# Performance work log

Measured on AMD Instinct MI355X. Metric: run time of the kernel, lower is better.

The kernel has to match this reference:

```python
import jax, jax.numpy as jnp
import numpy as np

N, C, H, W = 64, 512, 32, 32
HID, NCLS = 240, 10


def setup_inputs() -> dict:
    key = jax.random.key(0)
    ks = jax.random.split(key, 6)
    d = {
        "x": jax.random.normal(ks[0], (N, C, H, W), jnp.float32),
        "bn1_g": jnp.ones((C,), jnp.float32),
        "bn1_b": jnp.zeros((C,), jnp.float32),
        "bn1_m": jnp.zeros((C,), jnp.float32),
        "bn1_v": jnp.ones((C,), jnp.float32),
        "conv1_w": jax.random.normal(ks[1], (C, C, 3, 3), jnp.float32) * 0.02,
        "bn2_g": jnp.ones((C,), jnp.float32),
        "bn2_b": jnp.zeros((C,), jnp.float32),
        "bn2_m": jnp.zeros((C,), jnp.float32),
        "bn2_v": jnp.ones((C,), jnp.float32),
        "conv2_w": jax.random.normal(ks[2], (C, C, 3, 3), jnp.float32) * 0.02,
        "fc1_w": jax.random.normal(ks[3], (HID, C), jnp.float32) * 0.05,
        "fc1_b": jnp.zeros((HID,), jnp.float32),
        "fc2_w": jax.random.normal(ks[4], (NCLS, HID), jnp.float32) * 0.05,
        "fc2_b": jnp.zeros((NCLS,), jnp.float32),
    }
    return d


def _bn(x, g, b, m, v, eps=1e-5):
    # eval-mode BatchNorm2d, NCHW
    inv = g / jnp.sqrt(v + eps)
    return x * inv[None, :, None, None] + (b - m * inv)[None, :, None, None]


def _conv3(x, w):
    return jax.lax.conv_general_dilated(
        x, w, window_strides=(1, 1), padding="SAME",
        dimension_numbers=("NCHW", "OIHW", "NCHW"))


def _probe(feat, fc1_w, fc1_b, fc2_w, fc2_b):
    # Global_Avg_Flatten -> Linear -> Softplus(beta=5) -> Linear
    g = feat.mean(axis=(2, 3))                       # (N, C)
    h = jax.nn.softplus(5.0 * (g @ fc1_w.T + fc1_b)) / 5.0  # (N, HID)
    return h @ fc2_w.T + fc2_b                       # (N, NCLS)


def _get_mask(feat, fc1_w, fc1_b, fc2_w, fc2_b):
    # eval branch: sum of top-1 + top-2 logits, grad wrt (detached) feat
    feat_sg = jax.lax.stop_gradient(feat)

    def logit_sum(f_):
        logits = _probe(f_, fc1_w, fc1_b, fc2_w, fc2_b)
        idx = jax.lax.top_k(logits, 2)[1]            # (N, 2) int indices
        return jnp.take_along_axis(logits, idx, axis=1).sum()

    g = jax.grad(logit_sum)(feat_sg)                 # (N, C, H, W)
    # adaptive_avg_pool2d(.,1)*H*W == spatial sum
    s = g.sum(axis=(2, 3))                           # (N, C)
    m = jax.nn.softmax(s, axis=1) * 2.0
    return m[:, :, None, None]


def reference(x, bn1_g, bn1_b, bn1_m, bn1_v, conv1_w,
              bn2_g, bn2_b, bn2_m, bn2_v, conv2_w,
              fc1_w, fc1_b, fc2_w, fc2_b):
    out1 = jax.nn.relu(_bn(x, bn1_g, bn1_b, bn1_m, bn1_v))  # equalInOut path
    mask = _get_mask(out1, fc1_w, fc1_b, fc2_w, fc2_b)
    pred_probe = _probe(out1, fc1_w, fc1_b, fc2_w, fc2_b)
    masked = out1 * mask
    h = jax.nn.relu(_bn(_conv3(masked, conv1_w), bn2_g, bn2_b, bn2_m, bn2_v))
    h = _conv3(h, conv2_w)
    out = x + h
    return (out, pred_probe)
```

## Files before the change

### kernel.cpp

```cpp
#include <hip/hip_runtime.h>
#include <stdint.h>

typedef __bf16 bf16x8 __attribute__((ext_vector_type(8)));
typedef float f32x4v __attribute__((ext_vector_type(4)));

typedef __attribute__((address_space(1))) const void gconst_t;
typedef __attribute__((address_space(3))) void lds_t;

#define GLL16(gp, sp) __builtin_amdgcn_global_load_lds((gconst_t*)(uintptr_t)(gp), (lds_t*)(uintptr_t)(sp), 16, 0, 0)

__device__ __forceinline__ unsigned short f2bf(float f) {
  unsigned int u = __float_as_uint(f);
  u = (u + 0x7FFFu + ((u >> 16) & 1u)) >> 16;
  return (unsigned short)u;
}
__device__ __forceinline__ float bf2f(unsigned int b) {
  return __uint_as_float(b << 16);
}

#define SPP 1156

__global__ __launch_bounds__(512) void bnprep(
    const float* __restrict__ g1, const float* __restrict__ b1,
    const float* __restrict__ m1, const float* __restrict__ v1,
    const float* __restrict__ g2, const float* __restrict__ b2,
    const float* __restrict__ m2, const float* __restrict__ v2,
    float* __restrict__ bnp) {
  int t = threadIdx.x;
  float i1 = g1[t] * rsqrtf(v1[t] + 1e-5f);
  bnp[t] = i1;
  bnp[512 + t] = b1[t] - m1[t] * i1;
  float i2 = g2[t] * rsqrtf(v2[t] + 1e-5f);
  bnp[1024 + t] = i2;
  bnp[1536 + t] = b2[t] - m2[t] * i2;
}

__global__ __launch_bounds__(256) void ring_zero(unsigned short* __restrict__ Ap,
                                                 unsigned short* __restrict__ Hp) {
  const int n = blockIdx.y;
  const int p = blockIdx.x * 4 + (threadIdx.x >> 6);
  const int lane = threadIdx.x & 63;
  int y, x;
  if (p < 34) { y = 0; x = p; }
  else if (p < 68) { y = 33; x = p - 34; }
  else if (p < 100) { y = p - 67; x = 0; }
  else { y = p - 99; x = 33; }
  const uint4 z = {0u, 0u, 0u, 0u};
  const size_t off = ((size_t)((n * 34 + y) * 34 + x)) * 512 + lane * 8;
  *(uint4*)(Ap + off) = z;
  *(uint4*)(Hp + off) = z;
}

__global__ __launch_bounds__(256) void wtrans(const float* __restrict__ w1, const float* __restrict__ w2,
                                              unsigned short* __restrict__ w1t, unsigned short* __restrict__ w2t) {
  unsigned e = blockIdx.x * 256u + threadIdx.x;
  if (e >= 4718592u) return;
  const float* w = (e < 2359296u) ? w1 : w2;
  unsigned short* o = (e < 2359296u) ? w1t : w2t;
  unsigned r = (e < 2359296u) ? e : (e - 2359296u);
  unsigned ci = r & 511u, co = (r >> 9) & 511u, tt = r >> 18;
  o[r] = f2bf(w[(co * 512u + ci) * 9u + tt]);
}

__global__ __launch_bounds__(256) void bn1_relu_stage(const float* __restrict__ x, const float* __restrict__ bnp,
                                                      unsigned short* __restrict__ Ap, float* __restrict__ partial) {
  int bid = blockIdx.x;
  int n = bid >> 6, ciblk = (bid >> 3) & 7, yblk = bid & 7;
  int ci0 = ciblk * 64, y0 = yblk * 4;
  int t = threadIdx.x;
  __shared__ __align__(16) float vals[64 * 128];
  __shared__ float ivs[64], bbs[64];
  if (t < 64) { ivs[t] = bnp[ci0 + t]; bbs[t] = bnp[512 + ci0 + t]; }
  __syncthreads();
#pragma unroll
  for (int i = 0; i < 8; ++i) {
    int f4 = i * 256 + t;
    int cil = f4 >> 5, xq = f4 & 31;
    const float* src = x + ((size_t)(n * 512 + ci0 + cil)) * 1024 + y0 * 32 + xq * 4;
    f32x4v v = *(const f32x4v*)src;
    float iv = ivs[cil], bb = bbs[cil];
    f32x4v r;
    r[0] = fmaxf(fmaf(v[0], iv, bb), 0.f);
    r[1] = fmaxf(fmaf(v[1], iv, bb), 0.f);
    r[2] = fmaxf(fmaf(v[2], iv, bb), 0.f);
    r[3] = fmaxf(fmaf(v[3], iv, bb), 0.f);
    *(f32x4v*)&vals[cil * 128 + xq * 4] = r;
  }
  __syncthreads();
  {
    int cil = t >> 2, q = t & 3;
    float s = 0.f;
#pragma unroll
    for (int j = 0; j < 32; ++j) s += vals[cil * 128 + q * 32 + j];
    s += __shfl_xor(s, 1);
    s += __shfl_xor(s, 2);
    if (q == 0) partial[((size_t)n * 512 + ci0 + cil) * 8 + yblk] = s;
  }
  {
    int yx = t >> 1, half = t & 1;
    int y = y0 + (yx >> 5), xx = yx & 31;
    unsigned short* dp = Ap + ((size_t)((n * 34 + y + 1) * 34 + (xx + 1))) * 512 + ci0 + half * 32;
    unsigned wrd[16];
#pragma unroll
    for (int j = 0; j < 16; ++j) {
      unsigned lo = f2bf(vals[(half * 32 + 2 * j) * 128 + yx]);
      unsigned hi = f2bf(vals[(half * 32 + 2 * j + 1) * 128 + yx]);
      wrd[j] = lo | (hi << 16);
    }
#pragma unroll
    for (int k = 0; k < 4; ++k) {
      uint4 u;
      u.x = wrd[k * 4]; u.y = wrd[k * 4 + 1]; u.z = wrd[k * 4 + 2]; u.w = wrd[k * 4 + 3];
      *(uint4*)(dp + k * 8) = u;
    }
  }
}

__global__ __launch_bounds__(256) void probe_mask(const float* __restrict__ partial,
                                                  const float* __restrict__ fc1w, const float* __restrict__ fc1b,
                                                  const float* __restrict__ fc2w, const float* __restrict__ fc2b,
                                                  float* __restrict__ maskp, float* __restrict__ probeout) {
  int n = blockIdx.x, t = threadIdx.x;
  int lane = t & 63, wv = t >> 6;
  __shared__ float gl[512], sl[512], zl[240], hl[240], dzl[240], logl[10], red[4];
  __shared__ int idx2[2];
  for (int c = t; c < 512; c += 256) {
    const float* pp = partial + ((size_t)n * 512 + c) * 8;
    float s = 0.f;
#pragma unroll
    for (int j = 0; j < 8; ++j) s += pp[j];
    gl[c] = s * (1.f / 1024.f);
  }
  __syncthreads();
  if (t < 240) {
    float z = fc1b[t];
    const float* wr = fc1w + t * 512;
    for (int c = 0; c < 512; ++c) z = fmaf(gl[c], wr[c], z);
    zl[t] = z;
    float u = 5.f * z;
    float sp = (u > 20.f) ? u : log1pf(expf(u));
    hl[t] = sp * 0.2f;
  }
  __syncthreads();
  if (t < 10) {
    float L = fc2b[t];
    const float* wr = fc2w + t * 240;
    for (int h = 0; h < 240; ++h) L = fmaf(hl[h], wr[h], L);
    logl[t] = L;
    probeout[n * 10 + t] = L;
  }
  __syncthreads();
  if (t == 0) {
    float b1v = -1e30f, b2v = -1e30f; int i1 = 0, i2 = 0;
    for (int j = 0; j < 10; ++j) {
      float v = logl[j];
      if (v > b1v) { b2v = b1v; i2 = i1; b1v = v; i1 = j; }
      else if (v > b2v) { b2v = v; i2 = j; }
    }
    idx2[0] = i1; idx2[1] = i2;
  }
  __syncthreads();
  if (t < 240) {
    float dh = fc2w[idx2[0] * 240 + t] + fc2w[idx2[1] * 240 + t];
    float u = 5.f * zl[t];
    float sg = 1.f / (1.f + expf(-u));
    dzl[t] = dh * sg;
  }
  __syncthreads();
  for (int c = t; c < 512; c += 256) {
    float s = 0.f;
    for (int h = 0; h < 240; ++h) s = fmaf(dzl[h], fc1w[h * 512 + c], s);
    sl[c] = s;
  }
  __syncthreads();
  float m = fmaxf(sl[t], sl[t + 256]);
#pragma unroll
  for (int o = 32; o > 0; o >>= 1) m = fmaxf(m, __shfl_xor(m, o));
  if (lane == 0) red[wv] = m;
  __syncthreads();
  float mx = fmaxf(fmaxf(red[0], red[1]), fmaxf(red[2], red[3]));
  float e0 = expf(sl[t] - mx), e1 = expf(sl[t + 256] - mx);
  float sum = e0 + e1;
#pragma unroll
  for (int o = 32; o > 0; o >>= 1) sum += __shfl_xor(sum, o);
  __syncthreads();
  if (lane == 0) red[wv] = sum;
  __syncthreads();
  float inv = 2.f / (red[0] + red[1] + red[2] + red[3]);
  maskp[(size_t)n * 512 + t] = e0 * inv;
  maskp[(size_t)n * 512 + t + 256] = e1 * inv;
}

__global__ __launch_bounds__(256) void apply_mask(unsigned short* __restrict__ Ap, const float* __restrict__ maskp) {
  int n = blockIdx.y;
  size_t off = (size_t)n * (SPP * 512) + (size_t)blockIdx.x * 2048 + threadIdx.x * 8;
  int ci0 = (int)(threadIdx.x * 8) & 511;
  uint4 v = *(uint4*)(Ap + off);
  const float* mp = maskp + n * 512 + ci0;
  unsigned r0, r1;
  r0 = f2bf(bf2f(v.x & 0xFFFFu) * mp[0]); r1 = f2bf(bf2f(v.x >> 16) * mp[1]); v.x = r0 | (r1 << 16);
  r0 = f2bf(bf2f(v.y & 0xFFFFu) * mp[2]); r1 = f2bf(bf2f(v.y >> 16) * mp[3]); v.y = r0 | (r1 << 16);
  r0 = f2bf(bf2f(v.z & 0xFFFFu) * mp[4]); r1 = f2bf(bf2f(v.z >> 16) * mp[5]); v.z = r0 | (r1 << 16);
  r0 = f2bf(bf2f(v.w & 0xFFFFu) * mp[6]); r1 = f2bf(bf2f(v.w >> 16) * mp[7]); v.w = r0 | (r1 << 16);
  *(uint4*)(Ap + off) = v;
}

#define RD_A(QM, TAP) do {                                                    \
  const int _c0 = ((((QM) * 2 + (TAP) / 3) * 34 + (TAP) % 3)) * 128;          \
  const int _l0 = lterm[((((QM) * 2 + (TAP) / 3) * 34 + (TAP) % 3)) & 7];     \
  const int _c1 = _c0 + 8704;                                                 \
  const int _l1 = lterm[((((QM) * 2 + (TAP) / 3) * 34 + (TAP) % 3) + 4) & 7]; \
  a[0][0] = *(const bf16x8*)(ldsAW + _c0 + _l0);                              \
  a[0][1] = *(const bf16x8*)(ldsAW + _c0 + (_l0 ^ 64));                       \
  a[1][0] = *(const bf16x8*)(ldsAW + _c0 + 2048 + _l0);                       \
  a[1][1] = *(const bf16x8*)(ldsAW + _c0 + 2048 + (_l0 ^ 64));                \
  a[2][0] = *(const bf16x8*)(ldsAW + _c1 + _l1);                              \
  a[2][1] = *(const bf16x8*)(ldsAW + _c1 + (_l1 ^ 64));                       \
  a[3][0] = *(const bf16x8*)(ldsAW + _c1 + 2048 + _l1);                       \
  a[3][1] = *(const bf16x8*)(ldsAW + _c1 + 2048 + (_l1 ^ 64));                \
} while (0)

#define RD_B(QN, BUFR) do {                                                   \
  const int _b0 = 49152 + (BUFR) * 32768 + (QN) * 4096 + bRdC;                \
  _Pragma("unroll") for (int ni = 0; ni < 2; ++ni) {                          \
    b[QN][ni][0] = *(const bf16x8*)(ldsb + _b0 + ni * 2048);                  \
    b[QN][ni][1] = *(const bf16x8*)(ldsb + (_b0 ^ 64) + ni * 2048); }         \
} while (0)

#define ST_B(BUFW, H, BP) do {                                                \
  GLL16((BP) + bOff[H][0], ldsb + 49152 + (BUFW) * 32768 + (H) * 16384 + tb); \
  GLL16((BP) + bOff[H][1],                                                    \
        ldsb + 49152 + (BUFW) * 32768 + (H) * 16384 + 8192 + tb);             \
} while (0)

#define ST_A3(AP) do {                                                        \
  GLL16((AP) + aSrc[0], ldsb + tb);                                           \
  GLL16((AP) + aSrc[1], ldsb + 8192 + tb);                                    \
  GLL16((AP) + aSrc[2], ldsb + 16384 + tb);                                   \
  GLL16((AP) + aSrc[3], ldsb + 24576 + tb);                                   \
  GLL16((AP) + aSrc[4], ldsb + 32768 + tb);                                   \
  GLL16((AP) + aSrc[5], ldsb + 40960 + tb);                                   \
} while (0)

#define MFMA_Q(QM, QN) do {                                                   \
  _Pragma("unroll") for (int mi = 0; mi < 4; ++mi)                            \
  _Pragma("unroll") for (int ni = 0; ni < 2; ++ni) {                          \
    acc[QM][QN][mi][ni] = __builtin_amdgcn_mfma_f32_16x16x32_bf16(            \
        a[mi][0], b[QN][ni][0], acc[QM][QN][mi][ni], 0, 0, 0);                \
    acc[QM][QN][mi][ni] = __builtin_amdgcn_mfma_f32_16x16x32_bf16(            \
        a[mi][1], b[QN][ni][1], acc[QM][QN][mi][ni], 0, 0, 0); }              \
} while (0)

#define BARR __builtin_amdgcn_s_barrier()
#define LGKM0 do { asm volatile("s_waitcnt lgkmcnt(0)" ::: "memory");         \
                   __builtin_amdgcn_sched_barrier(0); } while (0)
#define VM4 asm volatile("s_waitcnt vmcnt(4)" ::: "memory")
#define VM0 asm volatile("s_waitcnt vmcnt(0)" ::: "memory")
#define PRIO1 __builtin_amdgcn_s_setprio(1)
#define PRIO0 __builtin_amdgcn_s_setprio(0)

#define TAPSTEP(TAP) do {                                                     \
  const unsigned short* _bp2;                                                 \
  if ((TAP) <= 6)      _bp2 = Wt + (size_t)((TAP) + 2) * 262144 + k8 * 64;    \
  else if ((TAP) == 7) _bp2 = (k8 < 7) ? Wt + (size_t)(k8 + 1) * 64           \
                                       : Wt + (size_t)8 * 262144 + 7 * 64;    \
  else                 _bp2 = (k8 < 7) ? Wt + 262144 + (size_t)(k8 + 1) * 64  \
                                       : Wt + (size_t)8 * 262144 + 7 * 64;    \
                                                                     \
  RD_A(0, TAP); RD_B(0, (TAP) % 3);                                           \
  ST_B(((TAP) + 2) % 3, 0, _bp2);                                             \
  BARR; LGKM0;                                                                \
  PRIO1; MFMA_Q(0, 0); PRIO0;                                                 \
  BARR;                                                                       \
                                                                     \
  RD_B(1, (TAP) % 3);                                                         \
  ST_B(((TAP) + 2) % 3, 1, _bp2);                                             \
  BARR; LGKM0;                                                                \
  PRIO1; MFMA_Q(0, 1); PRIO0;                                                 \
  BARR;                                                                       \
                                                                     \
  RD_A(1, TAP);                                                               \
  BARR; LGKM0;                                                                \
  if ((TAP) < 8) {                                                            \
    PRIO1; MFMA_Q(1, 1); MFMA_Q(1, 0); PRIO0;                                 \
    VM4; BARR;                                                                \
  } else {                                                                    \
    PRIO1; MFMA_Q(1, 1); PRIO0;                                               \
    BARR;                                                                     \
    if (k8 < 7) { ST_A3(Ag + (size_t)(k8 + 1) * 64); }                        \
    BARR;                                                                     \
    PRIO1; MFMA_Q(1, 0); PRIO0;                                               \
    VM0; BARR;                                                                \
  }                                                                           \
} while (0)

template <int MODE>
__global__ __launch_bounds__(512, 2) void conv256(
    const unsigned short* __restrict__ Ain,
    const unsigned short* __restrict__ Wt,
    const float* __restrict__ bnp,
    unsigned short* __restrict__ Hout,
    const float* __restrict__ xres,
    float* __restrict__ outp) {
  __shared__ __align__(16) char ldsb[147456];

  const int t = threadIdx.x;
  const int lane = t & 63;
  const int wv = t >> 6;
  const int wm = wv >> 2;
  const int wn = wv & 3;

  const int bid = blockIdx.x;
  const int swz = (bid & 7) * 64 + (bid >> 3);
  const int nt = swz & 1, mt = swz >> 1;
  const int n = mt >> 2, yblk = mt & 3;
  const int co0 = nt * 256;

  const unsigned short* Ag = Ain + (size_t)n * (SPP * 512);

  int bOff[2][2];
#pragma unroll
  for (int i = 0; i < 2; ++i) {
    const int c = i * 512 + t;
    const int lr = c >> 3;
    const int kq = (c & 7) ^ (lr & 7);
#pragma unroll
    for (int h = 0; h < 2; ++h)
      bOff[h][i] = (co0 + h * 128 + lr) * 512 + kq * 8;
  }
  int aSrc[6];
#pragma unroll
  for (int r = 0; r < 6; ++r) {
    const int s = r * 64 + (t >> 3);
    const int kq = (t & 7) ^ (s & 7);
    aSrc[r] = (yblk * 272 + s) * 512 + kq * 8;
  }
  const int tb = t * 16;
  const int k0 = ((lane >> 4) ^ (lane & 7)) << 4;
  int lterm[8];
#pragma unroll
  for (int m = 0; m < 8; ++m)
    lterm[m] = (lane & 15) * 128 + (((lane >> 4) ^ ((m + (lane & 15)) & 7)) << 4);
  const char* ldsAW = ldsb + wm * 17408;
  const int bRdC = (wn >> 1) * 16384 + (((wn & 1) << 6) + (lane & 15)) * 128 + k0;

  bf16x8 a[4][2];
  bf16x8 b[2][2][2];
  f32x4v acc[2][2][4][2];
  const f32x4v zero = {0.f, 0.f, 0.f, 0.f};
#pragma unroll
  for (int qm = 0; qm < 2; ++qm)
#pragma unroll
    for (int qn = 0; qn < 2; ++qn)
#pragma unroll
      for (int mi = 0; mi < 4; ++mi)
#pragma unroll
        for (int ni = 0; ni < 2; ++ni) acc[qm][qn][mi][ni] = zero;

  {
    ST_A3(Ag);
    ST_B(0, 0, Wt); ST_B(0, 1, Wt);
    ST_B(1, 0, Wt + 262144); ST_B(1, 1, Wt + 262144);
    VM0; BARR;
  }

  for (int k8 = 0; k8 < 8; ++k8) {
    TAPSTEP(0); TAPSTEP(1); TAPSTEP(2);
    TAPSTEP(3); TAPSTEP(4); TAPSTEP(5);
    TAPSTEP(6); TAPSTEP(7); TAPSTEP(8);
  }
  VM0;
  __syncthreads();

  if constexpr (MODE == 1) {
#pragma unroll
    for (int qn = 0; qn < 2; ++qn)
#pragma unroll
      for (int ni = 0; ni < 2; ++ni) {
        const int cog = co0 + wn * 64 + qn * 32 + ni * 16 + (lane & 15);
        const float iv = bnp[1024 + cog];
        const float bb = bnp[1536 + cog];
#pragma unroll
        for (int qm = 0; qm < 2; ++qm)
#pragma unroll
          for (int mi = 0; mi < 4; ++mi)
#pragma unroll
            for (int r = 0; r < 4; ++r) {
              const int row = wm * 128 + qm * 64 + mi * 16 + (lane >> 4) * 4 + r;
              const int y = yblk * 8 + (row >> 5), xx = row & 31;
              const float v = fmaxf(fmaf(acc[qm][qn][mi][ni][r], iv, bb), 0.f);
              Hout[((size_t)((n * 34 + y + 1) * 34 + (xx + 1))) * 512 + cog] = f2bf(v);
            }
      }
  } else {
    float* sm = (float*)ldsb;
    const int spat0 = yblk * 256;
#pragma unroll 1
    for (int h = 0; h < 4; ++h) {
      if (wn == h) {
#pragma unroll
        for (int qn = 0; qn < 2; ++qn)
#pragma unroll
          for (int ni = 0; ni < 2; ++ni)
#pragma unroll
            for (int qm = 0; qm < 2; ++qm)
#pragma unroll
              for (int mi = 0; mi < 4; ++mi)
#pragma unroll
                for (int r = 0; r < 4; ++r)
                  sm[(qn * 32 + ni * 16 + (lane & 15)) * 264 +
                     wm * 128 + qm * 64 + mi * 16 + (lane >> 4) * 4 + r] = acc[qm][qn][mi][ni][r];
      }
      __syncthreads();
#pragma unroll
      for (int j = 0; j < 8; ++j) {
        const int c = j * 512 + t;
        const int cc = c >> 6, px = (c & 63) * 4;
        f32x4v v = *(const f32x4v*)&sm[cc * 264 + px];
        const int cog = co0 + h * 64 + cc;
        const size_t o = ((size_t)(n * 512 + cog)) * 1024 + spat0 + px;
        const f32x4v xr = *(const f32x4v*)(xres + o);
        v = v + xr;
        *(f32x4v*)(outp + o) = v;
      }
      __syncthreads();
    }
  }
}

extern "C" void kernel_launch(void* const* d_in, const int* in_sizes, int n_in,
                              void* d_out, int out_size, void* d_ws, size_t ws_size,
                              hipStream_t stream) {
  (void)in_sizes; (void)n_in; (void)out_size; (void)ws_size;
  const float* x    = (const float*)d_in[0];
  const float* bn1g = (const float*)d_in[1];
  const float* bn1b = (const float*)d_in[2];
  const float* bn1m = (const float*)d_in[3];
  const float* bn1v = (const float*)d_in[4];
  const float* w1   = (const float*)d_in[5];
  const float* bn2g = (const float*)d_in[6];
  const float* bn2b = (const float*)d_in[7];
  const float* bn2m = (const float*)d_in[8];
  const float* bn2v = (const float*)d_in[9];
  const float* w2   = (const float*)d_in[10];
  const float* fc1w = (const float*)d_in[11];
  const float* fc1b = (const float*)d_in[12];
  const float* fc2w = (const float*)d_in[13];
  const float* fc2b = (const float*)d_in[14];

  float* out = (float*)d_out;
  float* probeo = out + (size_t)64 * 512 * 32 * 32;

  char* ws = (char*)d_ws;
  unsigned short* Ap  = (unsigned short*)(ws);
  unsigned short* Hp  = (unsigned short*)(ws + 75759616);
  unsigned short* W1t = (unsigned short*)(ws + 151519232);
  unsigned short* W2t = (unsigned short*)(ws + 156237824);
  float* partial      = (float*)(ws + 160956416);
  float* maskp        = (float*)(ws + 162004992);
  float* bnp          = (float*)(ws + 162136064);

  bnprep<<<1, 512, 0, stream>>>(bn1g, bn1b, bn1m, bn1v, bn2g, bn2b, bn2m, bn2v, bnp);
  ring_zero<<<dim3(33, 64), 256, 0, stream>>>(Ap, Hp);
  wtrans<<<18432, 256, 0, stream>>>(w1, w2, W1t, W2t);
  bn1_relu_stage<<<4096, 256, 0, stream>>>(x, bnp, Ap, partial);
  probe_mask<<<64, 256, 0, stream>>>(partial, fc1w, fc1b, fc2w, fc2b, maskp, probeo);
  apply_mask<<<dim3(289, 64), 256, 0, stream>>>(Ap, maskp);
  conv256<1><<<512, 512, 0, stream>>>(Ap, W1t, bnp, Hp, nullptr, nullptr);
  conv256<2><<<512, 512, 0, stream>>>(Hp, W2t, bnp, nullptr, x, out);
}
```

Before: 599.9 us.

## Halve conv output-channel tile to 128 and double-buffer weights for higher occupancy

Each conv block now covers 128 output channels instead of 256, and the launch doubles to 1024 blocks. Weight staging moves from a triple buffer to a double buffer, so LDS per block drops from 144KB to 80KB and the launch bound asks for more resident blocks. Accumulator registers are halved. In exchange the A (activation) tile is loaded twice as often, lowering reuse of A per MFMA, and the weight prefetch now waits on vmcnt(0) every tap, giving a shallower pipeline.

```diff
diff --git a/kernel.cpp b/kernel.cpp
--- a/kernel.cpp
+++ b/kernel.cpp
@@ -205,104 +205,111 @@
   *(uint4*)(Ap + off) = v;
 }
 
+#define LT(M) ((l4 ^ (((M) + l7) & 7)) << 4)
+
 #define RD_A(QM, TAP) do {                                                    \
-  const int _c0 = ((((QM) * 2 + (TAP) / 3) * 34 + (TAP) % 3)) * 128;          \
-  const int _l0 = lterm[((((QM) * 2 + (TAP) / 3) * 34 + (TAP) % 3)) & 7];     \
-  const int _c1 = _c0 + 8704;                                                 \
-  const int _l1 = lterm[((((QM) * 2 + (TAP) / 3) * 34 + (TAP) % 3) + 4) & 7]; \
-  a[0][0] = *(const bf16x8*)(ldsAW + _c0 + _l0);                              \
-  a[0][1] = *(const bf16x8*)(ldsAW + _c0 + (_l0 ^ 64));                       \
-  a[1][0] = *(const bf16x8*)(ldsAW + _c0 + 2048 + _l0);                       \
-  a[1][1] = *(const bf16x8*)(ldsAW + _c0 + 2048 + (_l0 ^ 64));                \
-  a[2][0] = *(const bf16x8*)(ldsAW + _c1 + _l1);                              \
-  a[2][1] = *(const bf16x8*)(ldsAW + _c1 + (_l1 ^ 64));                       \
-  a[3][0] = *(const bf16x8*)(ldsAW + _c1 + 2048 + _l1);                       \
-  a[3][1] = *(const bf16x8*)(ldsAW + _c1 + 2048 + (_l1 ^ 64));                \
-} while (0)
-
-#define RD_B(QN, BUFR) do {                                                   \
-  const int _b0 = 49152 + (BUFR) * 32768 + (QN) * 4096 + bRdC;                \
-  _Pragma("unroll") for (int ni = 0; ni < 2; ++ni) {                          \
-    b[QN][ni][0] = *(const bf16x8*)(ldsb + _b0 + ni * 2048);                  \
-    b[QN][ni][1] = *(const bf16x8*)(ldsb + (_b0 ^ 64) + ni * 2048); }         \
-} while (0)
-
-#define ST_B(BUFW, H, BP) do {                                                \
-  GLL16((BP) + bOff[H][0], ldsb + 49152 + (BUFW) * 32768 + (H) * 16384 + tb); \
-  GLL16((BP) + bOff[H][1],                                                    \
-        ldsb + 49152 + (BUFW) * 32768 + (H) * 16384 + 8192 + tb);             \
+  const int _S0 = ((QM) * 2 + (TAP) / 3) * 34 + (TAP) % 3;                    \
+  const int _l0 = l15x128 + LT(_S0 & 7);                                      \
+  const int _l1 = l15x128 + LT((_S0 + 4) & 7);                                \
+  const char* _p0 = ldsAW + _S0 * 128;                                        \
+  const char* _p1 = _p0 + 8704;                                               \
+  a[0][0] = *(const bf16x8*)(_p0 + _l0);                                      \
+  a[0][1] = *(const bf16x8*)(_p0 + (_l0 ^ 64));                               \
+  a[1][0] = *(const bf16x8*)(_p0 + 2048 + _l0);                               \
+  a[1][1] = *(const bf16x8*)(_p0 + 2048 + (_l0 ^ 64));                        \
+  a[2][0] = *(const bf16x8*)(_p1 + _l1);                                      \
+  a[2][1] = *(const bf16x8*)(_p1 + (_l1 ^ 64));                               \
+  a[3][0] = *(const bf16x8*)(_p1 + 2048 + _l1);                               \
+  a[3][1] = *(const bf16x8*)(_p1 + 2048 + (_l1 ^ 64));                        \
+} while (0)
+
+#define RD_B(BUF) do {                                                        \
+  const char* _pb = ldsb + 49152 + (BUF) * 16384 + bRdC;                      \
+  b[0][0] = *(const bf16x8*)(_pb);                                            \
+  b[0][1] = *(const bf16x8*)(ldsb + 49152 + (BUF) * 16384 + (bRdC ^ 64));     \
+  b[1][0] = *(const bf16x8*)(_pb + 2048);                                     \
+  b[1][1] = *(const bf16x8*)(ldsb + 49152 + (BUF) * 16384 + (bRdC ^ 64) + 2048); \
+} while (0)
+
+#define ST_B(BUF, BP) do {                                                    \
+  GLL16((BP) + bOff0,         ldsb + 49152 + (BUF) * 16384 + tb);             \
+  GLL16((BP) + bOff0 + 32768, ldsb + 49152 + (BUF) * 16384 + 8192 + tb);      \
 } while (0)
 
 #define ST_A3(AP) do {                                                        \
-  GLL16((AP) + aSrc[0], ldsb + tb);                                           \
-  GLL16((AP) + aSrc[1], ldsb + 8192 + tb);                                    \
-  GLL16((AP) + aSrc[2], ldsb + 16384 + tb);                                   \
-  GLL16((AP) + aSrc[3], ldsb + 24576 + tb);                                   \
-  GLL16((AP) + aSrc[4], ldsb + 32768 + tb);                                   \
-  GLL16((AP) + aSrc[5], ldsb + 40960 + tb);                                   \
-} while (0)
-
-#define MFMA_Q(QM, QN) do {                                                   \
+  GLL16((AP) + aOff0,          ldsb + tb);                                    \
+  GLL16((AP) + aOff0 + 32768,  ldsb + 8192 + tb);                             \
+  GLL16((AP) + aOff0 + 65536,  ldsb + 16384 + tb);                            \
+  GLL16((AP) + aOff0 + 98304,  ldsb + 24576 + tb);                            \
+  GLL16((AP) + aOff0 + 131072, ldsb + 32768 + tb);                            \
+  GLL16((AP) + aOff0 + 163840, ldsb + 40960 + tb);                            \
+} while (0)
+
+#define MFMA_H(QM) do {                                                       \
   _Pragma("unroll") for (int mi = 0; mi < 4; ++mi)                            \
   _Pragma("unroll") for (int ni = 0; ni < 2; ++ni) {                          \
-    acc[QM][QN][mi][ni] = __builtin_amdgcn_mfma_f32_16x16x32_bf16(            \
-        a[mi][0], b[QN][ni][0], acc[QM][QN][mi][ni], 0, 0, 0);                \
-    acc[QM][QN][mi][ni] = __builtin_amdgcn_mfma_f32_16x16x32_bf16(            \
-        a[mi][1], b[QN][ni][1], acc[QM][QN][mi][ni], 0, 0, 0); }              \
+    acc[QM][mi][ni] = __builtin_amdgcn_mfma_f32_16x16x32_bf16(                \
+        a[mi][0], b[ni][0], acc[QM][mi][ni], 0, 0, 0);                        \
+    acc[QM][mi][ni] = __builtin_amdgcn_mfma_f32_16x16x32_bf16(                \
+        a[mi][1], b[ni][1], acc[QM][mi][ni], 0, 0, 0); }                      \
+} while (0)
+
+#define MFMA_HN(QM, NI) do {                                                  \
+  _Pragma("unroll") for (int mi = 0; mi < 4; ++mi) {                          \
+    acc[QM][mi][NI] = __builtin_amdgcn_mfma_f32_16x16x32_bf16(                \
+        a[mi][0], b[NI][0], acc[QM][mi][NI], 0, 0, 0);                        \
+    acc[QM][mi][NI] = __builtin_amdgcn_mfma_f32_16x16x32_bf16(                \
+        a[mi][1], b[NI][1], acc[QM][mi][NI], 0, 0, 0); }                      \
 } while (0)
 
 #define BARR __builtin_amdgcn_s_barrier()
 #define LGKM0 do { asm volatile("s_waitcnt lgkmcnt(0)" ::: "memory");         \
                    __builtin_amdgcn_sched_barrier(0); } while (0)
-#define VM4 asm volatile("s_waitcnt vmcnt(4)" ::: "memory")
 #define VM0 asm volatile("s_waitcnt vmcnt(0)" ::: "memory")
 #define PRIO1 __builtin_amdgcn_s_setprio(1)
 #define PRIO0 __builtin_amdgcn_s_setprio(0)
 
-#define TAPSTEP(TAP) do {                                                     \
-  const unsigned short* _bp2;                                                 \
-  if ((TAP) <= 6)      _bp2 = Wt + (size_t)((TAP) + 2) * 262144 + k8 * 64;    \
-  else if ((TAP) == 7) _bp2 = (k8 < 7) ? Wt + (size_t)(k8 + 1) * 64           \
-                                       : Wt + (size_t)8 * 262144 + 7 * 64;    \
-  else                 _bp2 = (k8 < 7) ? Wt + 262144 + (size_t)(k8 + 1) * 64  \
-                                       : Wt + (size_t)8 * 262144 + 7 * 64;    \
+#define TAPSTEP(TAP, PAR) do {                                                \
+  const unsigned short* _bpn;                                                 \
+  if ((TAP) < 8) _bpn = Wt + (size_t)((TAP) + 1) * 262144 + k8 * 64;          \
+  else           _bpn = (k8 < 7) ? Wt + (size_t)(k8 + 1) * 64                 \
+                                 : Wt + (size_t)8 * 262144 + 7 * 64;          \
                                                                      \
-  RD_A(0, TAP); RD_B(0, (TAP) % 3);                                           \
-  ST_B(((TAP) + 2) % 3, 0, _bp2);                                             \
+  RD_A(0, TAP); RD_B(((TAP) + (PAR)) & 1);                                    \
+  ST_B((((TAP) + (PAR)) & 1) ^ 1, _bpn);                                      \
   BARR; LGKM0;                                                                \
-  PRIO1; MFMA_Q(0, 0); PRIO0;                                                 \
-  BARR;                                                                       \
-                                                                     \
-  RD_B(1, (TAP) % 3);                                                         \
-  ST_B(((TAP) + 2) % 3, 1, _bp2);                                             \
-  BARR; LGKM0;                                                                \
-  PRIO1; MFMA_Q(0, 1); PRIO0;                                                 \
+  PRIO1; MFMA_H(0); PRIO0;                                                    \
   BARR;                                                                       \
                                                                      \
   RD_A(1, TAP);                                                               \
   BARR; LGKM0;                                                                \
   if ((TAP) < 8) {                                                            \
-    PRIO1; MFMA_Q(1, 1); MFMA_Q(1, 0); PRIO0;                                 \
-    VM4; BARR;                                                                \
+    PRIO1; MFMA_H(1); PRIO0;                                                  \
+    VM0; BARR;                                                                \
   } else {                                                                    \
-    PRIO1; MFMA_Q(1, 1); PRIO0;                                               \
+    PRIO1; MFMA_HN(1, 0); PRIO0;                                              \
     BARR;                                                                     \
     if (k8 < 7) { ST_A3(Ag + (size_t)(k8 + 1) * 64); }                        \
     BARR;                                                                     \
-    PRIO1; MFMA_Q(1, 0); PRIO0;                                               \
+    PRIO1; MFMA_HN(1, 1); PRIO0;                                              \
     VM0; BARR;                                                                \
   }                                                                           \
 } while (0)
 
+#define TAP9(PAR)                                                             \
+  TAPSTEP(0, PAR); TAPSTEP(1, PAR); TAPSTEP(2, PAR);                          \
+  TAPSTEP(3, PAR); TAPSTEP(4, PAR); TAPSTEP(5, PAR);                          \
+  TAPSTEP(6, PAR); TAPSTEP(7, PAR); TAPSTEP(8, PAR);
+
 template <int MODE>
-__global__ __launch_bounds__(512, 2) void conv256(
+__global__ __launch_bounds__(512, 4) void conv256(
     const unsigned short* __restrict__ Ain,
     const unsigned short* __restrict__ Wt,
     const float* __restrict__ bnp,
     unsigned short* __restrict__ Hout,
     const float* __restrict__ xres,
     float* __restrict__ outp) {
-  __shared__ __align__(16) char ldsb[147456];
+  __shared__ __align__(16) char ldsb[81920];
 
   const int t = threadIdx.x;
   const int lane = t & 63;
@@ -311,87 +318,70 @@
   const int wn = wv & 3;
 
   const int bid = blockIdx.x;
-  const int swz = (bid & 7) * 64 + (bid >> 3);
-  const int nt = swz & 1, mt = swz >> 1;
+  const int logical = (bid & 7) * 128 + (bid >> 3);
+  const int nt = logical & 3, mt = logical >> 2;
   const int n = mt >> 2, yblk = mt & 3;
-  const int co0 = nt * 256;
+  const int co0 = nt * 128;
 
   const unsigned short* Ag = Ain + (size_t)n * (SPP * 512);
 
-  int bOff[2][2];
-#pragma unroll
-  for (int i = 0; i < 2; ++i) {
-    const int c = i * 512 + t;
-    const int lr = c >> 3;
-    const int kq = (c & 7) ^ (lr & 7);
-#pragma unroll
-    for (int h = 0; h < 2; ++h)
-      bOff[h][i] = (co0 + h * 128 + lr) * 512 + kq * 8;
-  }
-  int aSrc[6];
-#pragma unroll
-  for (int r = 0; r < 6; ++r) {
-    const int s = r * 64 + (t >> 3);
-    const int kq = (t & 7) ^ (s & 7);
-    aSrc[r] = (yblk * 272 + s) * 512 + kq * 8;
-  }
+  const int kq8 = ((t & 7) ^ ((t >> 3) & 7)) * 8;
+  const int aOff0 = (yblk * 272 + (t >> 3)) * 512 + kq8;
+  const int bOff0 = (co0 + (t >> 3)) * 512 + kq8;
   const int tb = t * 16;
-  const int k0 = ((lane >> 4) ^ (lane & 7)) << 4;
-  int lterm[8];
-#pragma unroll
-  for (int m = 0; m < 8; ++m)
-    lterm[m] = (lane & 15) * 128 + (((lane >> 4) ^ ((m + (lane & 15)) & 7)) << 4);
+  const int l4 = lane >> 4, l7 = lane & 7;
+  const int l15x128 = (lane & 15) * 128;
   const char* ldsAW = ldsb + wm * 17408;
-  const int bRdC = (wn >> 1) * 16384 + (((wn & 1) << 6) + (lane & 15)) * 128 + k0;
+  const int bRdC = (wn * 32 + (lane & 15)) * 128 + (((lane >> 4) ^ (lane & 7)) << 4);
 
   bf16x8 a[4][2];
-  bf16x8 b[2][2][2];
-  f32x4v acc[2][2][4][2];
+  bf16x8 b[2][2];
+  f32x4v acc[2][4][2];
   const f32x4v zero = {0.f, 0.f, 0.f, 0.f};
 #pragma unroll
   for (int qm = 0; qm < 2; ++qm)
 #pragma unroll
-    for (int qn = 0; qn < 2; ++qn)
-#pragma unroll
-      for (int mi = 0; mi < 4; ++mi)
-#pragma unroll
-        for (int ni = 0; ni < 2; ++ni) acc[qm][qn][mi][ni] = zero;
+    for (int mi = 0; mi < 4; ++mi)
+#pragma unroll
+      for (int ni = 0; ni < 2; ++ni) acc[qm][mi][ni] = zero;
 
   {
     ST_A3(Ag);
-    ST_B(0, 0, Wt); ST_B(0, 1, Wt);
-    ST_B(1, 0, Wt + 262144); ST_B(1, 1, Wt + 262144);
+    ST_B(0, Wt);
     VM0; BARR;
   }
 
-  for (int k8 = 0; k8 < 8; ++k8) {
-    TAPSTEP(0); TAPSTEP(1); TAPSTEP(2);
-    TAPSTEP(3); TAPSTEP(4); TAPSTEP(5);
-    TAPSTEP(6); TAPSTEP(7); TAPSTEP(8);
+  for (int k2 = 0; k2 < 4; ++k2) {
+    {
+      const int k8 = 2 * k2;
+      TAP9(0)
+    }
+    {
+      const int k8 = 2 * k2 + 1;
+      TAP9(1)
+    }
   }
   VM0;
   __syncthreads();
 
   if constexpr (MODE == 1) {
 #pragma unroll
-    for (int qn = 0; qn < 2; ++qn)
-#pragma unroll
-      for (int ni = 0; ni < 2; ++ni) {
-        const int cog = co0 + wn * 64 + qn * 32 + ni * 16 + (lane & 15);
-        const float iv = bnp[1024 + cog];
-        const float bb = bnp[1536 + cog];
-#pragma unroll
-        for (int qm = 0; qm < 2; ++qm)
-#pragma unroll
-          for (int mi = 0; mi < 4; ++mi)
-#pragma unroll
-            for (int r = 0; r < 4; ++r) {
-              const int row = wm * 128 + qm * 64 + mi * 16 + (lane >> 4) * 4 + r;
-              const int y = yblk * 8 + (row >> 5), xx = row & 31;
-              const float v = fmaxf(fmaf(acc[qm][qn][mi][ni][r], iv, bb), 0.f);
-              Hout[((size_t)((n * 34 + y + 1) * 34 + (xx + 1))) * 512 + cog] = f2bf(v);
-            }
-      }
+    for (int ni = 0; ni < 2; ++ni) {
+      const int cog = co0 + wn * 32 + ni * 16 + (lane & 15);
+      const float iv = bnp[1024 + cog];
+      const float bb = bnp[1536 + cog];
+#pragma unroll
+      for (int qm = 0; qm < 2; ++qm)
+#pragma unroll
+        for (int mi = 0; mi < 4; ++mi)
+#pragma unroll
+          for (int r = 0; r < 4; ++r) {
+            const int row = wm * 128 + qm * 64 + mi * 16 + (lane >> 4) * 4 + r;
+            const int y = yblk * 8 + (row >> 5), xx = row & 31;
+            const float v = fmaxf(fmaf(acc[qm][mi][ni][r], iv, bb), 0.f);
+            Hout[((size_t)((n * 34 + y + 1) * 34 + (xx + 1))) * 512 + cog] = f2bf(v);
+          }
+    }
   } else {
     float* sm = (float*)ldsb;
     const int spat0 = yblk * 256;
@@ -399,25 +389,23 @@
     for (int h = 0; h < 4; ++h) {
       if (wn == h) {
 #pragma unroll
-        for (int qn = 0; qn < 2; ++qn)
-#pragma unroll
-          for (int ni = 0; ni < 2; ++ni)
-#pragma unroll
-            for (int qm = 0; qm < 2; ++qm)
-#pragma unroll
-              for (int mi = 0; mi < 4; ++mi)
-#pragma unroll
-                for (int r = 0; r < 4; ++r)
-                  sm[(qn * 32 + ni * 16 + (lane & 15)) * 264 +
-                     wm * 128 + qm * 64 + mi * 16 + (lane >> 4) * 4 + r] = acc[qm][qn][mi][ni][r];
+        for (int ni = 0; ni < 2; ++ni)
+#pragma unroll
+          for (int qm = 0; qm < 2; ++qm)
+#pragma unroll
+            for (int mi = 0; mi < 4; ++mi)
+#pragma unroll
+              for (int r = 0; r < 4; ++r)
+                sm[(ni * 16 + (lane & 15)) * 264 +
+                   wm * 128 + qm * 64 + mi * 16 + (lane >> 4) * 4 + r] = acc[qm][mi][ni][r];
       }
       __syncthreads();
 #pragma unroll
-      for (int j = 0; j < 8; ++j) {
+      for (int j = 0; j < 4; ++j) {
         const int c = j * 512 + t;
         const int cc = c >> 6, px = (c & 63) * 4;
         f32x4v v = *(const f32x4v*)&sm[cc * 264 + px];
-        const int cog = co0 + h * 64 + cc;
+        const int cog = co0 + h * 32 + cc;
         const size_t o = ((size_t)(n * 512 + cog)) * 1024 + spat0 + px;
         const f32x4v xr = *(const f32x4v*)(xres + o);
         v = v + xr;
@@ -466,6 +454,6 @@
   bn1_relu_stage<<<4096, 256, 0, stream>>>(x, bnp, Ap, partial);
   probe_mask<<<64, 256, 0, stream>>>(partial, fc1w, fc1b, fc2w, fc2b, maskp, probeo);
   apply_mask<<<dim3(289, 64), 256, 0, stream>>>(Ap, maskp);
-  conv256<1><<<512, 512, 0, stream>>>(Ap, W1t, bnp, Hp, nullptr, nullptr);
-  conv256<2><<<512, 512, 0, stream>>>(Hp, W2t, bnp, nullptr, x, out);
-}
+  conv256<1><<<1024, 512, 0, stream>>>(Ap, W1t, bnp, Hp, nullptr, nullptr);
+  conv256<2><<<1024, 512, 0, stream>>>(Hp, W2t, bnp, nullptr, x, out);
+}
```

Result: slower. 830.2 us (+38.4%).
